# Optimization experiments

Hardware: AMD Instinct MI355X
Metric: run time of the kernel (lower is better)

Reference implementation:

```python
import jax, jax.numpy as jnp
import numpy as np

N, E = 50000, 1600000
FEAT, HID, HEADS = 256, 64, 2
NEG_SLOPE = 0.2


def gat_conv(x, src, dst, W, att_src, att_dst, bias, heads, out_ch):
    """PyG GATConv (concat=True, self-loops already appended to src/dst)."""
    n = x.shape[0]
    h = (x @ W).reshape(n, heads, out_ch)                      # [N,H,C]
    a_src = jnp.einsum('nhc,hc->nh', h, att_src)               # [N,H]
    a_dst = jnp.einsum('nhc,hc->nh', h, att_dst)               # [N,H]
    alpha = jax.nn.leaky_relu(a_src[src] + a_dst[dst], NEG_SLOPE)  # [E',H]
    # segment softmax over incoming edges of each dst node
    amax = jax.ops.segment_max(alpha, dst, num_segments=n)
    alpha = jnp.exp(alpha - amax[dst])
    denom = jax.ops.segment_sum(alpha, dst, num_segments=n)
    alpha = alpha / (denom[dst] + 1e-16)
    msg = h[src] * alpha[..., None]                            # [E',H,C]
    out = jax.ops.segment_sum(msg, dst, num_segments=n)        # [N,H,C]
    return out.reshape(n, heads * out_ch) + bias


def setup_inputs() -> dict:
    key = jax.random.key(0)
    ks = jax.random.split(key, 10)
    x = jax.random.normal(ks[0], (N, FEAT), dtype=jnp.float32)
    edge_index = jax.random.randint(ks[1], (2, E), 0, N, dtype=jnp.int64)
    s1 = 1.0 / np.sqrt(FEAT)
    s2 = 1.0 / np.sqrt(HID * HEADS)
    sa = 1.0 / np.sqrt(HID)
    return {
        'x': x,
        'edge_index': edge_index,
        'W1': jax.random.uniform(ks[2], (FEAT, HEADS * HID), jnp.float32, -s1, s1),
        'att_src1': jax.random.uniform(ks[3], (HEADS, HID), jnp.float32, -sa, sa),
        'att_dst1': jax.random.uniform(ks[4], (HEADS, HID), jnp.float32, -sa, sa),
        'b1': jnp.zeros((HEADS * HID,), jnp.float32),
        'W2': jax.random.uniform(ks[5], (HEADS * HID, HID), jnp.float32, -s2, s2),
        'att_src2': jax.random.uniform(ks[6], (1, HID), jnp.float32, -sa, sa),
        'att_dst2': jax.random.uniform(ks[7], (1, HID), jnp.float32, -sa, sa),
        'b2': jnp.zeros((HID,), jnp.float32),
    }


def reference(x, edge_index, W1, att_src1, att_dst1, b1, W2, att_src2, att_dst2, b2):
    n = x.shape[0]
    loop = jnp.arange(n, dtype=edge_index.dtype)
    src = jnp.concatenate([edge_index[0], loop])   # add self loops (PyG default)
    dst = jnp.concatenate([edge_index[1], loop])
    h = gat_conv(x, src, dst, W1, att_src1, att_dst1, b1, HEADS, HID)
    h = jax.nn.relu(h)  # dropout is identity in eval mode
    h = gat_conv(h, src, dst, W2, att_src2, att_dst2, b2, 1, HID)
    return jax.nn.log_softmax(h, axis=1)
```

## Files before the change

kernel.cpp:

```cpp
#include <hip/hip_runtime.h>
#include <hip/hip_bf16.h>
#include <math.h>

typedef short bf16x8 __attribute__((ext_vector_type(8)));
typedef float f32x4 __attribute__((ext_vector_type(4)));

#define BSHIFT 7
#define BWIDTH 128
#define PCHUNK 4096

__global__ void prep_kernel(int* __restrict__ bcnt,
                            const float* __restrict__ W1, const float* __restrict__ W2,
                            __hip_bfloat16* __restrict__ W1t,
                            __hip_bfloat16* __restrict__ W2t) {
    if (blockIdx.x == 0) {
        bcnt[threadIdx.x] = 0;
        bcnt[threadIdx.x + 256] = 0;
        return;
    }
    int idx = (blockIdx.x - 1) * 256 + threadIdx.x;
    const int n1 = 128 * 256;
    if (idx < n1) {
        int nn = idx >> 8, kk = idx & 255;
        W1t[idx] = __float2bfloat16(W1[kk * 128 + nn]);
    } else {
        int j = idx - n1;
        if (j < 64 * 128) {
            int nn = j >> 7, kk = j & 127;
            W2t[j] = __float2bfloat16(W2[kk * 64 + nn]);
        }
    }
}

__global__ __launch_bounds__(256) void bucket_hist(const int* __restrict__ ei, int E,
                                                   int* __restrict__ bcnt) {
    __shared__ int h[512];
    int tid = threadIdx.x;
    for (int i = tid; i < 512; i += 256) h[i] = 0;
    __syncthreads();
    int start = blockIdx.x * PCHUNK;
    int cnt = min(PCHUNK, E - start);
    for (int i = tid; i < cnt; i += 256)
        atomicAdd(&h[ei[E + start + i] >> BSHIFT], 1);
    __syncthreads();
    for (int i = tid; i < 512; i += 256)
        if (h[i]) atomicAdd(&bcnt[i], h[i]);
}

__global__ __launch_bounds__(512) void bucket_scan(const int* __restrict__ bcnt,
                                                   int* __restrict__ bbase,
                                                   int* __restrict__ bcur,
                                                   int nbk, int n) {
    __shared__ int s[512];
    int tid = threadIdx.x;
    int nodes = 0;
    if (tid < nbk) nodes = min(BWIDTH, n - (tid << BSHIFT));
    int v = (tid < nbk) ? bcnt[tid] + nodes : 0;
    s[tid] = v;
    __syncthreads();
    #pragma unroll
    for (int o = 1; o < 512; o <<= 1) {
        int t = (tid >= o) ? s[tid - o] : 0;
        __syncthreads();
        s[tid] += t;
        __syncthreads();
    }
    if (tid < nbk) {
        int ex = s[tid] - v;
        bbase[tid] = ex;
        bcur[tid] = ex - (tid << BSHIFT);
    }
    if (tid == nbk) bbase[nbk] = s[tid];
}

__global__ __launch_bounds__(256) void partition_edges(const int* __restrict__ ei, int E,
                                                       int* __restrict__ bcur,
                                                       int* __restrict__ tmp) {
    __shared__ int2 stage[PCHUNK];
    __shared__ int h[512];
    __shared__ int lbase[512];
    int tid = threadIdx.x;
    int start = blockIdx.x * PCHUNK;
    int cnt = min(PCHUNK, E - start);
    for (int i = tid; i < 512; i += 256) h[i] = 0;
    __syncthreads();
    for (int i = tid; i < cnt; i += 256) {
        int s = ei[start + i];
        int d = ei[E + start + i];
        stage[i] = make_int2(s, d);
        atomicAdd(&h[d >> BSHIFT], 1);
    }
    __syncthreads();
    for (int i = tid; i < 512; i += 256) {
        if (h[i] > 0) lbase[i] = atomicAdd(&bcur[i], h[i]);
        h[i] = 0;
    }
    __syncthreads();
    for (int i = tid; i < cnt; i += 256) {
        int2 e = stage[i];
        int b = e.y >> BSHIFT;
        int r = atomicAdd(&h[b], 1);
        tmp[lbase[b] + r] = (e.x << BSHIFT) | (e.y & (BWIDTH - 1));
    }
}

__global__ __launch_bounds__(256) void bucket_csr(const int* __restrict__ bbase,
                                                  const int* __restrict__ tmp,
                                                  int* __restrict__ offs,
                                                  int* __restrict__ srcs,
                                                  int n, int nbk) {
    __shared__ int cnt[BWIDTH];
    __shared__ int sa[BWIDTH];
    __shared__ int cur[BWIDTH];
    int b = blockIdx.x;
    int tid = threadIdx.x;
    int node0 = b << BSHIFT;
    int nnodes = min(BWIDTH, n - node0);
    int cb = bbase[b];
    int ce = bbase[b + 1];
    int tb = cb - node0;
    int ecnt = (ce - cb) - nnodes;

    if (tid < BWIDTH) cnt[tid] = (tid < nnodes) ? 1 : 0;
    __syncthreads();
    for (int i = tid; i < ecnt; i += 256)
        atomicAdd(&cnt[tmp[tb + i] & (BWIDTH - 1)], 1);
    __syncthreads();
    if (tid < BWIDTH) sa[tid] = cnt[tid];
    __syncthreads();
    #pragma unroll
    for (int o = 1; o < BWIDTH; o <<= 1) {
        int v = 0;
        if (tid < BWIDTH) { v = sa[tid]; if (tid >= o) v += sa[tid - o]; }
        __syncthreads();
        if (tid < BWIDTH) sa[tid] = v;
        __syncthreads();
    }
    if (tid < BWIDTH) {
        int ex = sa[tid] - cnt[tid];
        if (tid < nnodes) {
            offs[node0 + tid] = cb + ex;
            srcs[cb + ex] = node0 + tid;
        }
        cur[tid] = ex + (tid < nnodes ? 1 : 0);
    }
    if (b == nbk - 1 && tid == 0) offs[n] = ce;
    __syncthreads();
    for (int i = tid; i < ecnt; i += 256) {
        int e = tmp[tb + i];
        int li = e & (BWIDTH - 1);
        int r = atomicAdd(&cur[li], 1);
        srcs[cb + r] = e >> BSHIFT;
    }
}

template <bool A_BF16, int NT, int HEADS, int KSTEPS>
__global__ __launch_bounds__(256) void gemm_att(
    const void* __restrict__ Av, const __hip_bfloat16* __restrict__ Bt,
    __hip_bfloat16* __restrict__ C,
    const float* __restrict__ atts, const float* __restrict__ attd,
    float* __restrict__ a_s, float* __restrict__ a_d, int M) {
    constexpr int K = KSTEPS * 32;
    constexpr int N = NT * 16;
    constexpr int KH = 128;
    constexpr int NCH = (K + KH - 1) / KH;
    constexpr int LDB = KH + 8;
    __shared__ __hip_bfloat16 Bs[N][LDB];

    int tid = threadIdx.x;
    int w = tid >> 6, l = tid & 63;
    int q = l >> 4, m16 = l & 15;
    int bm = blockIdx.x * 64;
    int arow = bm + w * 16 + m16;
    if (arow >= M) arow = M - 1;

    f32x4 acc[NT];
    #pragma unroll
    for (int t = 0; t < NT; t++) acc[t] = (f32x4){0.f, 0.f, 0.f, 0.f};

    #pragma unroll
    for (int ch = 0; ch < NCH; ch++) {
        const int cb = ch * KH;
        bf16x8 af[4];
        float4 st[8];
        if (A_BF16) {
            const __hip_bfloat16* A = (const __hip_bfloat16*)Av + (size_t)arow * K + cb + q * 8;
            #pragma unroll
            for (int t = 0; t < 4; t++)
                af[t] = *(const bf16x8*)(A + t * 32);
        } else {
            const float* A = (const float*)Av + (size_t)arow * K + cb + q * 8;
            #pragma unroll
            for (int t = 0; t < 4; t++) {
                st[2 * t]     = *(const float4*)(A + t * 32);
                st[2 * t + 1] = *(const float4*)(A + t * 32 + 4);
            }
        }
        for (int i = tid; i < (N * KH) / 8; i += 256) {
            int row = i >> 4;
            int k = (i & 15) * 8;
            *(uint4*)&Bs[row][k] = *(const uint4*)(Bt + (size_t)row * K + cb + k);
        }
        __syncthreads();
        if (!A_BF16) {
            #pragma unroll
            for (int t = 0; t < 4; t++) {
                union { __hip_bfloat16 h[8]; bf16x8 v; } u;
                float4 v0 = st[2 * t], v1 = st[2 * t + 1];
                u.h[0] = __float2bfloat16(v0.x); u.h[1] = __float2bfloat16(v0.y);
                u.h[2] = __float2bfloat16(v0.z); u.h[3] = __float2bfloat16(v0.w);
                u.h[4] = __float2bfloat16(v1.x); u.h[5] = __float2bfloat16(v1.y);
                u.h[6] = __float2bfloat16(v1.z); u.h[7] = __float2bfloat16(v1.w);
                af[t] = u.v;
            }
        }
        #pragma unroll
        for (int t = 0; t < 4; t++) {
            #pragma unroll
            for (int c = 0; c < NT; c++) {
                bf16x8 b = *(const bf16x8*)&Bs[c * 16 + m16][t * 32 + q * 8];
                acc[c] = __builtin_amdgcn_mfma_f32_16x16x32_bf16(af[t], b, acc[c], 0, 0, 0);
            }
        }
        if (ch + 1 < NCH) __syncthreads();
    }

    #pragma unroll
    for (int t = 0; t < NT; t++) {
        #pragma unroll
        for (int r = 0; r < 4; r++) {
            int row = bm + w * 16 + q * 4 + r;
            if (row < M) C[(size_t)row * N + t * 16 + m16] = __float2bfloat16(acc[t][r]);
        }
    }

    float ps[HEADS][4], pd[HEADS][4];
    #pragma unroll
    for (int hh = 0; hh < HEADS; hh++)
        #pragma unroll
        for (int r = 0; r < 4; r++) { ps[hh][r] = 0.f; pd[hh][r] = 0.f; }
    #pragma unroll
    for (int t = 0; t < NT; t++) {
        int ch = t * 16 + m16;
        float asw = atts[ch], adw = attd[ch];
        int hh = (HEADS == 2) ? (t >> 2) : 0;
        #pragma unroll
        for (int r = 0; r < 4; r++) {
            ps[hh][r] = fmaf(acc[t][r], asw, ps[hh][r]);
            pd[hh][r] = fmaf(acc[t][r], adw, pd[hh][r]);
        }
    }
    #pragma unroll
    for (int o = 1; o < 16; o <<= 1) {
        #pragma unroll
        for (int hh = 0; hh < HEADS; hh++)
            #pragma unroll
            for (int r = 0; r < 4; r++) {
                ps[hh][r] += __shfl_xor(ps[hh][r], o);
                pd[hh][r] += __shfl_xor(pd[hh][r], o);
            }
    }
    if (m16 == 0) {
        #pragma unroll
        for (int r = 0; r < 4; r++) {
            int row = bm + w * 16 + q * 4 + r;
            if (row < M) {
                if (HEADS == 2) {
                    a_s[row * 2]     = ps[0][r];
                    a_s[row * 2 + 1] = ps[1][r];
                    a_d[row * 2]     = pd[0][r];
                    a_d[row * 2 + 1] = pd[1][r];
                } else {
                    a_s[row] = ps[0][r];
                    a_d[row] = pd[0][r];
                }
            }
        }
    }
}

__device__ __forceinline__ float leaky(float r) {
    return r < 0.f ? 0.2f * r : r;
}

__device__ __forceinline__ void unpack2(unsigned u, float& lo, float& hi) {
    lo = __uint_as_float(u << 16);
    hi = __uint_as_float(u & 0xffff0000u);
}

__global__ __launch_bounds__(256) void edge_agg_l1(
    const int* __restrict__ offs, const int* __restrict__ srcs,
    const __hip_bfloat16* __restrict__ h1, const float* __restrict__ asv,
    const float* __restrict__ adv, const float* __restrict__ bias,
    __hip_bfloat16* __restrict__ out, int d0, int dlim) {
    int d = d0 + ((blockIdx.x * blockDim.x + threadIdx.x) >> 6);
    int lane = threadIdx.x & 63;
    if (d >= dlim) return;
    int start = offs[d], end = offs[d + 1];
    float ad0 = adv[2 * d], ad1 = adv[2 * d + 1];

    int sub = lane & 15;
    int g = lane >> 4;
    int ch0 = sub * 8;
    int hsel = sub >> 3;

    float s0 = 0.f, s1 = 0.f;
    float acc[8];
    #pragma unroll
    for (int k = 0; k < 8; k++) acc[k] = 0.f;

    for (int base = start; base < end; base += 64) {
        int cnt = min(64, end - base);
        int s_l = 0;
        float e0 = 0.f, e1 = 0.f;
        if (lane < cnt) {
            s_l = srcs[base + lane];
            float2 a = *(const float2*)(asv + 2 * s_l);
            e0 = __expf(leaky(a.x + ad0));
            e1 = __expf(leaky(a.y + ad1));
        }
        s0 += e0;
        s1 += e1;

        int steps = (cnt + 3) >> 2;
        int jj = 0;
        for (; jj + 4 <= steps; jj += 4) {
            float wgt[4]; int sr[4];
            #pragma unroll
            for (int u = 0; u < 4; u++) {
                int e = (jj + u) * 4 + g;
                float w0 = __shfl(e0, e);
                float w1 = __shfl(e1, e);
                sr[u] = __shfl(s_l, e);
                wgt[u] = hsel ? w1 : w0;
            }
            uint4 v[4];
            #pragma unroll
            for (int u = 0; u < 4; u++)
                v[u] = *(const uint4*)(h1 + (size_t)sr[u] * 128 + ch0);
            #pragma unroll
            for (int u = 0; u < 4; u++) {
                float f0, f1, f2, f3, f4, f5, f6, f7;
                unpack2(v[u].x, f0, f1); unpack2(v[u].y, f2, f3);
                unpack2(v[u].z, f4, f5); unpack2(v[u].w, f6, f7);
                float wA = wgt[u];
                acc[0] = fmaf(wA, f0, acc[0]); acc[1] = fmaf(wA, f1, acc[1]);
                acc[2] = fmaf(wA, f2, acc[2]); acc[3] = fmaf(wA, f3, acc[3]);
                acc[4] = fmaf(wA, f4, acc[4]); acc[5] = fmaf(wA, f5, acc[5]);
                acc[6] = fmaf(wA, f6, acc[6]); acc[7] = fmaf(wA, f7, acc[7]);
            }
        }
        for (; jj + 2 <= steps; jj += 2) {
            int eA = jj * 4 + g, eB = eA + 4;
            float w0A = __shfl(e0, eA), w1A = __shfl(e1, eA);
            int sA = __shfl(s_l, eA);
            float w0B = __shfl(e0, eB), w1B = __shfl(e1, eB);
            int sB = __shfl(s_l, eB);
            float wA = hsel ? w1A : w0A;
            float wB = hsel ? w1B : w0B;
            uint4 vA = *(const uint4*)(h1 + (size_t)sA * 128 + ch0);
            uint4 vB = *(const uint4*)(h1 + (size_t)sB * 128 + ch0);
            float f0, f1, f2, f3, f4, f5, f6, f7;
            unpack2(vA.x, f0, f1); unpack2(vA.y, f2, f3);
            unpack2(vA.z, f4, f5); unpack2(vA.w, f6, f7);
            acc[0] = fmaf(wA, f0, acc[0]); acc[1] = fmaf(wA, f1, acc[1]);
            acc[2] = fmaf(wA, f2, acc[2]); acc[3] = fmaf(wA, f3, acc[3]);
            acc[4] = fmaf(wA, f4, acc[4]); acc[5] = fmaf(wA, f5, acc[5]);
            acc[6] = fmaf(wA, f6, acc[6]); acc[7] = fmaf(wA, f7, acc[7]);
            unpack2(vB.x, f0, f1); unpack2(vB.y, f2, f3);
            unpack2(vB.z, f4, f5); unpack2(vB.w, f6, f7);
            acc[0] = fmaf(wB, f0, acc[0]); acc[1] = fmaf(wB, f1, acc[1]);
            acc[2] = fmaf(wB, f2, acc[2]); acc[3] = fmaf(wB, f3, acc[3]);
            acc[4] = fmaf(wB, f4, acc[4]); acc[5] = fmaf(wB, f5, acc[5]);
            acc[6] = fmaf(wB, f6, acc[6]); acc[7] = fmaf(wB, f7, acc[7]);
        }
        if (jj < steps) {
            int eA = jj * 4 + g;
            float w0A = __shfl(e0, eA), w1A = __shfl(e1, eA);
            int sA = __shfl(s_l, eA);
            float wA = hsel ? w1A : w0A;
            uint4 vA = *(const uint4*)(h1 + (size_t)sA * 128 + ch0);
            float f0, f1, f2, f3, f4, f5, f6, f7;
            unpack2(vA.x, f0, f1); unpack2(vA.y, f2, f3);
            unpack2(vA.z, f4, f5); unpack2(vA.w, f6, f7);
            acc[0] = fmaf(wA, f0, acc[0]); acc[1] = fmaf(wA, f1, acc[1]);
            acc[2] = fmaf(wA, f2, acc[2]); acc[3] = fmaf(wA, f3, acc[3]);
            acc[4] = fmaf(wA, f4, acc[4]); acc[5] = fmaf(wA, f5, acc[5]);
            acc[6] = fmaf(wA, f6, acc[6]); acc[7] = fmaf(wA, f7, acc[7]);
        }
    }
    #pragma unroll
    for (int o = 16; o < 64; o <<= 1)
        #pragma unroll
        for (int k = 0; k < 8; k++) acc[k] += __shfl_xor(acc[k], o);
    #pragma unroll
    for (int o = 1; o < 64; o <<= 1) {
        s0 += __shfl_xor(s0, o);
        s1 += __shfl_xor(s1, o);
    }

    if (lane < 16) {
        float invh = 1.f / ((hsel ? s1 : s0) + 1e-16f);
        float4 b0 = *(const float4*)(bias + ch0);
        float4 b1 = *(const float4*)(bias + ch0 + 4);
        union { __hip_bfloat16 h[8]; uint4 u; } o2;
        o2.h[0] = __float2bfloat16(fmaxf(fmaf(acc[0], invh, b0.x), 0.f));
        o2.h[1] = __float2bfloat16(fmaxf(fmaf(acc[1], invh, b0.y), 0.f));
        o2.h[2] = __float2bfloat16(fmaxf(fmaf(acc[2], invh, b0.z), 0.f));
        o2.h[3] = __float2bfloat16(fmaxf(fmaf(acc[3], invh, b0.w), 0.f));
        o2.h[4] = __float2bfloat16(fmaxf(fmaf(acc[4], invh, b1.x), 0.f));
        o2.h[5] = __float2bfloat16(fmaxf(fmaf(acc[5], invh, b1.y), 0.f));
        o2.h[6] = __float2bfloat16(fmaxf(fmaf(acc[6], invh, b1.z), 0.f));
        o2.h[7] = __float2bfloat16(fmaxf(fmaf(acc[7], invh, b1.w), 0.f));
        *(uint4*)(out + (size_t)d * 128 + ch0) = o2.u;
    }
}

__global__ __launch_bounds__(256) void edge_agg_l2(
    const int* __restrict__ offs, const int* __restrict__ srcs,
    const __hip_bfloat16* __restrict__ h2, const float* __restrict__ asv,
    const float* __restrict__ adv, const float* __restrict__ bias,
    float* __restrict__ out, int n) {
    int d = (blockIdx.x * blockDim.x + threadIdx.x) >> 6;
    int lane = threadIdx.x & 63;
    if (d >= n) return;
    int start = offs[d], end = offs[d + 1];
    float ad = adv[d];

    int sub = lane & 7;
    int g = lane >> 3;
    int ch0 = sub * 8;

    float ssum = 0.f;
    float acc[8];
    #pragma unroll
    for (int k = 0; k < 8; k++) acc[k] = 0.f;

    for (int base = start; base < end; base += 64) {
        int cnt = min(64, end - base);
        int s_l = 0;
        float ew = 0.f;
        if (lane < cnt) {
            s_l = srcs[base + lane];
            ew = __expf(leaky(asv[s_l] + ad));
        }
        ssum += ew;

        int steps = (cnt + 7) >> 3;
        int jj = 0;
        for (; jj + 4 <= steps; jj += 4) {
            float wgt[4]; int sr[4];
            #pragma unroll
            for (int u = 0; u < 4; u++) {
                int e = (jj + u) * 8 + g;
                wgt[u] = __shfl(ew, e);
                sr[u] = __shfl(s_l, e);
            }
            uint4 v[4];
            #pragma unroll
            for (int u = 0; u < 4; u++)
                v[u] = *(const uint4*)(h2 + (size_t)sr[u] * 64 + ch0);
            #pragma unroll
            for (int u = 0; u < 4; u++) {
                float f0, f1, f2, f3, f4, f5, f6, f7;
                unpack2(v[u].x, f0, f1); unpack2(v[u].y, f2, f3);
                unpack2(v[u].z, f4, f5); unpack2(v[u].w, f6, f7);
                float wA = wgt[u];
                acc[0] = fmaf(wA, f0, acc[0]); acc[1] = fmaf(wA, f1, acc[1]);
                acc[2] = fmaf(wA, f2, acc[2]); acc[3] = fmaf(wA, f3, acc[3]);
                acc[4] = fmaf(wA, f4, acc[4]); acc[5] = fmaf(wA, f5, acc[5]);
                acc[6] = fmaf(wA, f6, acc[6]); acc[7] = fmaf(wA, f7, acc[7]);
            }
        }
        for (; jj + 2 <= steps; jj += 2) {
            int eA = jj * 8 + g, eB = eA + 8;
            float wA = __shfl(ew, eA);
            int sA = __shfl(s_l, eA);
            float wB = __shfl(ew, eB);
            int sB = __shfl(s_l, eB);
            uint4 vA = *(const uint4*)(h2 + (size_t)sA * 64 + ch0);
            uint4 vB = *(const uint4*)(h2 + (size_t)sB * 64 + ch0);
            float f0, f1, f2, f3, f4, f5, f6, f7;
            unpack2(vA.x, f0, f1); unpack2(vA.y, f2, f3);
            unpack2(vA.z, f4, f5); unpack2(vA.w, f6, f7);
            acc[0] = fmaf(wA, f0, acc[0]); acc[1] = fmaf(wA, f1, acc[1]);
            acc[2] = fmaf(wA, f2, acc[2]); acc[3] = fmaf(wA, f3, acc[3]);
            acc[4] = fmaf(wA, f4, acc[4]); acc[5] = fmaf(wA, f5, acc[5]);
            acc[6] = fmaf(wA, f6, acc[6]); acc[7] = fmaf(wA, f7, acc[7]);
            unpack2(vB.x, f0, f1); unpack2(vB.y, f2, f3);
            unpack2(vB.z, f4, f5); unpack2(vB.w, f6, f7);
            acc[0] = fmaf(wB, f0, acc[0]); acc[1] = fmaf(wB, f1, acc[1]);
            acc[2] = fmaf(wB, f2, acc[2]); acc[3] = fmaf(wB, f3, acc[3]);
            acc[4] = fmaf(wB, f4, acc[4]); acc[5] = fmaf(wB, f5, acc[5]);
            acc[6] = fmaf(wB, f6, acc[6]); acc[7] = fmaf(wB, f7, acc[7]);
        }
        if (jj < steps) {
            int eA = jj * 8 + g;
            float wA = __shfl(ew, eA);
            int sA = __shfl(s_l, eA);
            uint4 vA = *(const uint4*)(h2 + (size_t)sA * 64 + ch0);
            float f0, f1, f2, f3, f4, f5, f6, f7;
            unpack2(vA.x, f0, f1); unpack2(vA.y, f2, f3);
            unpack2(vA.z, f4, f5); unpack2(vA.w, f6, f7);
            acc[0] = fmaf(wA, f0, acc[0]); acc[1] = fmaf(wA, f1, acc[1]);
            acc[2] = fmaf(wA, f2, acc[2]); acc[3] = fmaf(wA, f3, acc[3]);
            acc[4] = fmaf(wA, f4, acc[4]); acc[5] = fmaf(wA, f5, acc[5]);
            acc[6] = fmaf(wA, f6, acc[6]); acc[7] = fmaf(wA, f7, acc[7]);
        }
    }
    #pragma unroll
    for (int o = 8; o < 64; o <<= 1)
        #pragma unroll
        for (int k = 0; k < 8; k++) acc[k] += __shfl_xor(acc[k], o);
    #pragma unroll
    for (int o = 1; o < 64; o <<= 1) ssum += __shfl_xor(ssum, o);

    float inv = 1.f / (ssum + 1e-16f);
    float4 b0 = *(const float4*)(bias + ch0);
    float4 b1 = *(const float4*)(bias + ch0 + 4);
    float v[8];
    v[0] = fmaf(acc[0], inv, b0.x); v[1] = fmaf(acc[1], inv, b0.y);
    v[2] = fmaf(acc[2], inv, b0.z); v[3] = fmaf(acc[3], inv, b0.w);
    v[4] = fmaf(acc[4], inv, b1.x); v[5] = fmaf(acc[5], inv, b1.y);
    v[6] = fmaf(acc[6], inv, b1.z); v[7] = fmaf(acc[7], inv, b1.w);

    float vm = v[0];
    #pragma unroll
    for (int k = 1; k < 8; k++) vm = fmaxf(vm, v[k]);
    #pragma unroll
    for (int o = 1; o < 8; o <<= 1) vm = fmaxf(vm, __shfl_xor(vm, o));
    float se_loc = 0.f;
    #pragma unroll
    for (int k = 0; k < 8; k++) se_loc += __expf(v[k] - vm);
    #pragma unroll
    for (int o = 1; o < 8; o <<= 1) se_loc += __shfl_xor(se_loc, o);
    float lse = vm + logf(se_loc);

    if (lane < 8) {
        float4 o0 = make_float4(v[0] - lse, v[1] - lse, v[2] - lse, v[3] - lse);
        float4 o1 = make_float4(v[4] - lse, v[5] - lse, v[6] - lse, v[7] - lse);
        *(float4*)(out + (size_t)d * 64 + ch0) = o0;
        *(float4*)(out + (size_t)d * 64 + ch0 + 4) = o1;
    }
}

extern "C" void kernel_launch(void* const* d_in, const int* in_sizes, int n_in,
                              void* d_out, int out_size, void* d_ws, size_t ws_size,
                              hipStream_t stream) {
    const float* x    = (const float*)d_in[0];
    const int*   ei   = (const int*)d_in[1];
    const float* W1   = (const float*)d_in[2];
    const float* as1w = (const float*)d_in[3];
    const float* ad1w = (const float*)d_in[4];
    const float* b1   = (const float*)d_in[5];
    const float* W2   = (const float*)d_in[6];
    const float* as2w = (const float*)d_in[7];
    const float* ad2w = (const float*)d_in[8];
    const float* b2   = (const float*)d_in[9];
    float* out = (float*)d_out;

    const int n = in_sizes[0] / 256;
    const int E = in_sizes[1] / 2;
    const int tot = E + n;
    const int nbk = (n + BWIDTH - 1) / BWIDTH;

    char* p = (char*)d_ws;
    auto alloc = [&](size_t bytes) {
        void* r = (void*)p;
        p += (bytes + 255) & ~(size_t)255;
        return r;
    };
    int*   offs  = (int*)alloc((size_t)(n + 1) * 4);
    int*   srcs  = (int*)alloc((size_t)tot * 4);
    int*   tmp   = (int*)alloc((size_t)E * 4);
    int*   bcnt  = (int*)alloc(512 * 4);
    int*   bbase = (int*)alloc(512 * 4);
    int*   bcur  = (int*)alloc(512 * 4);
    __hip_bfloat16* W1t = (__hip_bfloat16*)alloc((size_t)128 * 256 * 2);
    __hip_bfloat16* W2t = (__hip_bfloat16*)alloc((size_t)64 * 128 * 2);
    __hip_bfloat16* h1  = (__hip_bfloat16*)alloc((size_t)n * 128 * 2);
    __hip_bfloat16* out1= (__hip_bfloat16*)alloc((size_t)n * 128 * 2);
    __hip_bfloat16* h2  = (__hip_bfloat16*)alloc((size_t)n * 64 * 2);
    float* a_s1 = (float*)alloc((size_t)n * 2 * 4);
    float* a_d1 = (float*)alloc((size_t)n * 2 * 4);
    float* a_s2 = (float*)alloc((size_t)n * 4);
    float* a_d2 = (float*)alloc((size_t)n * 4);

    int pblocks = (E + PCHUNK - 1) / PCHUNK;

    prep_kernel<<<1 + (128 * 256 + 64 * 128 + 255) / 256, 256, 0, stream>>>(
        bcnt, W1, W2, W1t, W2t);

    bucket_hist<<<pblocks, 256, 0, stream>>>(ei, E, bcnt);
    bucket_scan<<<1, 512, 0, stream>>>(bcnt, bbase, bcur, nbk, n);
    partition_edges<<<pblocks, 256, 0, stream>>>(ei, E, bcur, tmp);
    bucket_csr<<<nbk, 256, 0, stream>>>(bbase, tmp, offs, srcs, n, nbk);

    gemm_att<false, 8, 2, 8><<<(n + 63) / 64, 256, 0, stream>>>(
        x, W1t, h1, as1w, ad1w, a_s1, a_d1, n);
    int nh = n / 2;
    edge_agg_l1<<<((size_t)nh * 64 + 255) / 256, 256, 0, stream>>>(
        offs, srcs, h1, a_s1, a_d1, b1, out1, 0, nh);
    edge_agg_l1<<<((size_t)(n - nh) * 64 + 255) / 256, 256, 0, stream>>>(
        offs, srcs, h1, a_s1, a_d1, b1, out1, nh, n);

    gemm_att<true, 4, 1, 4><<<(n + 63) / 64, 256, 0, stream>>>(
        out1, W2t, h2, as2w, ad2w, a_s2, a_d2, n);
    edge_agg_l2<<<((size_t)n * 64 + 255) / 256, 256, 0, stream>>>(
        offs, srcs, h2, a_s2, a_d2, b2, out, n);
}
```

Before: 268.4 us.

## Compute edge weights per lane and prefetch source indices in GAT aggregation

Both edge aggregation kernels drop the cooperative load-then-shuffle scheme. Each lane group now reads its own source indices directly, prefetching the next four a loop iteration ahead, and computes the attention exponent redundantly for its own edges, keeping only a partial denominator per group. This removes the shuffle traffic and the 64-edge chunk serialization, at the cost of redundant exp/asv loads across the channel lanes of a group. The layer-1 aggregation is also merged back into a single launch instead of two half launches.

```diff
diff --git a/kernel.cpp b/kernel.cpp
--- a/kernel.cpp
+++ b/kernel.cpp
@@ -292,115 +292,114 @@
     const int* __restrict__ offs, const int* __restrict__ srcs,
     const __hip_bfloat16* __restrict__ h1, const float* __restrict__ asv,
     const float* __restrict__ adv, const float* __restrict__ bias,
-    __hip_bfloat16* __restrict__ out, int d0, int dlim) {
-    int d = d0 + ((blockIdx.x * blockDim.x + threadIdx.x) >> 6);
+    __hip_bfloat16* __restrict__ out, int n) {
+    int d = (blockIdx.x * blockDim.x + threadIdx.x) >> 6;
     int lane = threadIdx.x & 63;
-    if (d >= dlim) return;
+    if (d >= n) return;
     int start = offs[d], end = offs[d + 1];
-    float ad0 = adv[2 * d], ad1 = adv[2 * d + 1];
-
+    int cnt = end - start;
     int sub = lane & 15;
     int g = lane >> 4;
     int ch0 = sub * 8;
     int hsel = sub >> 3;
-
-    float s0 = 0.f, s1 = 0.f;
+    float ad = adv[2 * d + hsel];
+
+    float wsum = 0.f;
     float acc[8];
     #pragma unroll
     for (int k = 0; k < 8; k++) acc[k] = 0.f;
 
-    for (int base = start; base < end; base += 64) {
-        int cnt = min(64, end - base);
-        int s_l = 0;
-        float e0 = 0.f, e1 = 0.f;
-        if (lane < cnt) {
-            s_l = srcs[base + lane];
-            float2 a = *(const float2*)(asv + 2 * s_l);
-            e0 = __expf(leaky(a.x + ad0));
-            e1 = __expf(leaky(a.y + ad1));
-        }
-        s0 += e0;
-        s1 += e1;
-
-        int steps = (cnt + 3) >> 2;
-        int jj = 0;
-        for (; jj + 4 <= steps; jj += 4) {
-            float wgt[4]; int sr[4];
-            #pragma unroll
-            for (int u = 0; u < 4; u++) {
-                int e = (jj + u) * 4 + g;
-                float w0 = __shfl(e0, e);
-                float w1 = __shfl(e1, e);
-                sr[u] = __shfl(s_l, e);
-                wgt[u] = hsel ? w1 : w0;
-            }
-            uint4 v[4];
-            #pragma unroll
-            for (int u = 0; u < 4; u++)
-                v[u] = *(const uint4*)(h1 + (size_t)sr[u] * 128 + ch0);
-            #pragma unroll
-            for (int u = 0; u < 4; u++) {
-                float f0, f1, f2, f3, f4, f5, f6, f7;
-                unpack2(v[u].x, f0, f1); unpack2(v[u].y, f2, f3);
-                unpack2(v[u].z, f4, f5); unpack2(v[u].w, f6, f7);
-                float wA = wgt[u];
-                acc[0] = fmaf(wA, f0, acc[0]); acc[1] = fmaf(wA, f1, acc[1]);
-                acc[2] = fmaf(wA, f2, acc[2]); acc[3] = fmaf(wA, f3, acc[3]);
-                acc[4] = fmaf(wA, f4, acc[4]); acc[5] = fmaf(wA, f5, acc[5]);
-                acc[6] = fmaf(wA, f6, acc[6]); acc[7] = fmaf(wA, f7, acc[7]);
-            }
-        }
-        for (; jj + 2 <= steps; jj += 2) {
-            int eA = jj * 4 + g, eB = eA + 4;
-            float w0A = __shfl(e0, eA), w1A = __shfl(e1, eA);
-            int sA = __shfl(s_l, eA);
-            float w0B = __shfl(e0, eB), w1B = __shfl(e1, eB);
-            int sB = __shfl(s_l, eB);
-            float wA = hsel ? w1A : w0A;
-            float wB = hsel ? w1B : w0B;
-            uint4 vA = *(const uint4*)(h1 + (size_t)sA * 128 + ch0);
-            uint4 vB = *(const uint4*)(h1 + (size_t)sB * 128 + ch0);
-            float f0, f1, f2, f3, f4, f5, f6, f7;
-            unpack2(vA.x, f0, f1); unpack2(vA.y, f2, f3);
-            unpack2(vA.z, f4, f5); unpack2(vA.w, f6, f7);
-            acc[0] = fmaf(wA, f0, acc[0]); acc[1] = fmaf(wA, f1, acc[1]);
-            acc[2] = fmaf(wA, f2, acc[2]); acc[3] = fmaf(wA, f3, acc[3]);
-            acc[4] = fmaf(wA, f4, acc[4]); acc[5] = fmaf(wA, f5, acc[5]);
-            acc[6] = fmaf(wA, f6, acc[6]); acc[7] = fmaf(wA, f7, acc[7]);
-            unpack2(vB.x, f0, f1); unpack2(vB.y, f2, f3);
-            unpack2(vB.z, f4, f5); unpack2(vB.w, f6, f7);
-            acc[0] = fmaf(wB, f0, acc[0]); acc[1] = fmaf(wB, f1, acc[1]);
-            acc[2] = fmaf(wB, f2, acc[2]); acc[3] = fmaf(wB, f3, acc[3]);
-            acc[4] = fmaf(wB, f4, acc[4]); acc[5] = fmaf(wB, f5, acc[5]);
-            acc[6] = fmaf(wB, f6, acc[6]); acc[7] = fmaf(wB, f7, acc[7]);
-        }
-        if (jj < steps) {
-            int eA = jj * 4 + g;
-            float w0A = __shfl(e0, eA), w1A = __shfl(e1, eA);
-            int sA = __shfl(s_l, eA);
-            float wA = hsel ? w1A : w0A;
-            uint4 vA = *(const uint4*)(h1 + (size_t)sA * 128 + ch0);
-            float f0, f1, f2, f3, f4, f5, f6, f7;
-            unpack2(vA.x, f0, f1); unpack2(vA.y, f2, f3);
-            unpack2(vA.z, f4, f5); unpack2(vA.w, f6, f7);
-            acc[0] = fmaf(wA, f0, acc[0]); acc[1] = fmaf(wA, f1, acc[1]);
-            acc[2] = fmaf(wA, f2, acc[2]); acc[3] = fmaf(wA, f3, acc[3]);
-            acc[4] = fmaf(wA, f4, acc[4]); acc[5] = fmaf(wA, f5, acc[5]);
-            acc[6] = fmaf(wA, f6, acc[6]); acc[7] = fmaf(wA, f7, acc[7]);
-        }
-    }
-    #pragma unroll
-    for (int o = 16; o < 64; o <<= 1)
+    int full = cnt >> 2;
+    int ib = start + g;
+    int jj = 0;
+    int pA = 0, pB = 0, pC = 0, pD = 0;
+    if (jj + 4 <= full) {
+        pA = srcs[ib];      pB = srcs[ib + 4];
+        pC = srcs[ib + 8];  pD = srcs[ib + 12];
+    }
+    for (; jj + 4 <= full; jj += 4) {
+        int sA = pA, sB = pB, sC = pC, sD = pD;
+        if (jj + 8 <= full) {
+            int nb = ib + (jj + 4) * 4;
+            pA = srcs[nb];      pB = srcs[nb + 4];
+            pC = srcs[nb + 8];  pD = srcs[nb + 12];
+        }
+        uint4 vA = *(const uint4*)(h1 + (size_t)sA * 128 + ch0);
+        uint4 vB = *(const uint4*)(h1 + (size_t)sB * 128 + ch0);
+        uint4 vC = *(const uint4*)(h1 + (size_t)sC * 128 + ch0);
+        uint4 vD = *(const uint4*)(h1 + (size_t)sD * 128 + ch0);
+        float aA = asv[2 * sA + hsel];
+        float aB = asv[2 * sB + hsel];
+        float aC = asv[2 * sC + hsel];
+        float aD = asv[2 * sD + hsel];
+        float wA = __expf(leaky(aA + ad));
+        float wB = __expf(leaky(aB + ad));
+        float wC = __expf(leaky(aC + ad));
+        float wD = __expf(leaky(aD + ad));
+        wsum += (wA + wB) + (wC + wD);
+        float f0, f1, f2, f3, f4, f5, f6, f7;
+        unpack2(vA.x, f0, f1); unpack2(vA.y, f2, f3);
+        unpack2(vA.z, f4, f5); unpack2(vA.w, f6, f7);
+        acc[0] = fmaf(wA, f0, acc[0]); acc[1] = fmaf(wA, f1, acc[1]);
+        acc[2] = fmaf(wA, f2, acc[2]); acc[3] = fmaf(wA, f3, acc[3]);
+        acc[4] = fmaf(wA, f4, acc[4]); acc[5] = fmaf(wA, f5, acc[5]);
+        acc[6] = fmaf(wA, f6, acc[6]); acc[7] = fmaf(wA, f7, acc[7]);
+        unpack2(vB.x, f0, f1); unpack2(vB.y, f2, f3);
+        unpack2(vB.z, f4, f5); unpack2(vB.w, f6, f7);
+        acc[0] = fmaf(wB, f0, acc[0]); acc[1] = fmaf(wB, f1, acc[1]);
+        acc[2] = fmaf(wB, f2, acc[2]); acc[3] = fmaf(wB, f3, acc[3]);
+        acc[4] = fmaf(wB, f4, acc[4]); acc[5] = fmaf(wB, f5, acc[5]);
+        acc[6] = fmaf(wB, f6, acc[6]); acc[7] = fmaf(wB, f7, acc[7]);
+        unpack2(vC.x, f0, f1); unpack2(vC.y, f2, f3);
+        unpack2(vC.z, f4, f5); unpack2(vC.w, f6, f7);
+        acc[0] = fmaf(wC, f0, acc[0]); acc[1] = fmaf(wC, f1, acc[1]);
+        acc[2] = fmaf(wC, f2, acc[2]); acc[3] = fmaf(wC, f3, acc[3]);
+        acc[4] = fmaf(wC, f4, acc[4]); acc[5] = fmaf(wC, f5, acc[5]);
+        acc[6] = fmaf(wC, f6, acc[6]); acc[7] = fmaf(wC, f7, acc[7]);
+        unpack2(vD.x, f0, f1); unpack2(vD.y, f2, f3);
+        unpack2(vD.z, f4, f5); unpack2(vD.w, f6, f7);
+        acc[0] = fmaf(wD, f0, acc[0]); acc[1] = fmaf(wD, f1, acc[1]);
+        acc[2] = fmaf(wD, f2, acc[2]); acc[3] = fmaf(wD, f3, acc[3]);
+        acc[4] = fmaf(wD, f4, acc[4]); acc[5] = fmaf(wD, f5, acc[5]);
+        acc[6] = fmaf(wD, f6, acc[6]); acc[7] = fmaf(wD, f7, acc[7]);
+    }
+    for (; jj < full; jj++) {
+        int s = srcs[ib + jj * 4];
+        uint4 v = *(const uint4*)(h1 + (size_t)s * 128 + ch0);
+        float a = asv[2 * s + hsel];
+        float wA = __expf(leaky(a + ad));
+        wsum += wA;
+        float f0, f1, f2, f3, f4, f5, f6, f7;
+        unpack2(v.x, f0, f1); unpack2(v.y, f2, f3);
+        unpack2(v.z, f4, f5); unpack2(v.w, f6, f7);
+        acc[0] = fmaf(wA, f0, acc[0]); acc[1] = fmaf(wA, f1, acc[1]);
+        acc[2] = fmaf(wA, f2, acc[2]); acc[3] = fmaf(wA, f3, acc[3]);
+        acc[4] = fmaf(wA, f4, acc[4]); acc[5] = fmaf(wA, f5, acc[5]);
+        acc[6] = fmaf(wA, f6, acc[6]); acc[7] = fmaf(wA, f7, acc[7]);
+    }
+    if (full * 4 + g < cnt) {
+        int s = srcs[ib + full * 4];
+        uint4 v = *(const uint4*)(h1 + (size_t)s * 128 + ch0);
+        float a = asv[2 * s + hsel];
+        float wA = __expf(leaky(a + ad));
+        wsum += wA;
+        float f0, f1, f2, f3, f4, f5, f6, f7;
+        unpack2(v.x, f0, f1); unpack2(v.y, f2, f3);
+        unpack2(v.z, f4, f5); unpack2(v.w, f6, f7);
+        acc[0] = fmaf(wA, f0, acc[0]); acc[1] = fmaf(wA, f1, acc[1]);
+        acc[2] = fmaf(wA, f2, acc[2]); acc[3] = fmaf(wA, f3, acc[3]);
+        acc[4] = fmaf(wA, f4, acc[4]); acc[5] = fmaf(wA, f5, acc[5]);
+        acc[6] = fmaf(wA, f6, acc[6]); acc[7] = fmaf(wA, f7, acc[7]);
+    }
+    #pragma unroll
+    for (int o = 16; o < 64; o <<= 1) {
         #pragma unroll
         for (int k = 0; k < 8; k++) acc[k] += __shfl_xor(acc[k], o);
-    #pragma unroll
-    for (int o = 1; o < 64; o <<= 1) {
-        s0 += __shfl_xor(s0, o);
-        s1 += __shfl_xor(s1, o);
+        wsum += __shfl_xor(wsum, o);
     }
 
     if (lane < 16) {
-        float invh = 1.f / ((hsel ? s1 : s0) + 1e-16f);
+        float invh = 1.f / (wsum + 1e-16f);
         float4 b0 = *(const float4*)(bias + ch0);
         float4 b1 = *(const float4*)(bias + ch0 + 4);
         union { __hip_bfloat16 h[8]; uint4 u; } o2;
@@ -425,97 +424,104 @@
     int lane = threadIdx.x & 63;
     if (d >= n) return;
     int start = offs[d], end = offs[d + 1];
-    float ad = adv[d];
-
+    int cnt = end - start;
     int sub = lane & 7;
     int g = lane >> 3;
     int ch0 = sub * 8;
-
-    float ssum = 0.f;
+    float ad = adv[d];
+
+    float wsum = 0.f;
     float acc[8];
     #pragma unroll
     for (int k = 0; k < 8; k++) acc[k] = 0.f;
 
-    for (int base = start; base < end; base += 64) {
-        int cnt = min(64, end - base);
-        int s_l = 0;
-        float ew = 0.f;
-        if (lane < cnt) {
-            s_l = srcs[base + lane];
-            ew = __expf(leaky(asv[s_l] + ad));
-        }
-        ssum += ew;
-
-        int steps = (cnt + 7) >> 3;
-        int jj = 0;
-        for (; jj + 4 <= steps; jj += 4) {
-            float wgt[4]; int sr[4];
-            #pragma unroll
-            for (int u = 0; u < 4; u++) {
-                int e = (jj + u) * 8 + g;
-                wgt[u] = __shfl(ew, e);
-                sr[u] = __shfl(s_l, e);
-            }
-            uint4 v[4];
-            #pragma unroll
-            for (int u = 0; u < 4; u++)
-                v[u] = *(const uint4*)(h2 + (size_t)sr[u] * 64 + ch0);
-            #pragma unroll
-            for (int u = 0; u < 4; u++) {
-                float f0, f1, f2, f3, f4, f5, f6, f7;
-                unpack2(v[u].x, f0, f1); unpack2(v[u].y, f2, f3);
-                unpack2(v[u].z, f4, f5); unpack2(v[u].w, f6, f7);
-                float wA = wgt[u];
-                acc[0] = fmaf(wA, f0, acc[0]); acc[1] = fmaf(wA, f1, acc[1]);
-                acc[2] = fmaf(wA, f2, acc[2]); acc[3] = fmaf(wA, f3, acc[3]);
-                acc[4] = fmaf(wA, f4, acc[4]); acc[5] = fmaf(wA, f5, acc[5]);
-                acc[6] = fmaf(wA, f6, acc[6]); acc[7] = fmaf(wA, f7, acc[7]);
-            }
-        }
-        for (; jj + 2 <= steps; jj += 2) {
-            int eA = jj * 8 + g, eB = eA + 8;
-            float wA = __shfl(ew, eA);
-            int sA = __shfl(s_l, eA);
-            float wB = __shfl(ew, eB);
-            int sB = __shfl(s_l, eB);
-            uint4 vA = *(const uint4*)(h2 + (size_t)sA * 64 + ch0);
-            uint4 vB = *(const uint4*)(h2 + (size_t)sB * 64 + ch0);
-            float f0, f1, f2, f3, f4, f5, f6, f7;
-            unpack2(vA.x, f0, f1); unpack2(vA.y, f2, f3);
-            unpack2(vA.z, f4, f5); unpack2(vA.w, f6, f7);
-            acc[0] = fmaf(wA, f0, acc[0]); acc[1] = fmaf(wA, f1, acc[1]);
-            acc[2] = fmaf(wA, f2, acc[2]); acc[3] = fmaf(wA, f3, acc[3]);
-            acc[4] = fmaf(wA, f4, acc[4]); acc[5] = fmaf(wA, f5, acc[5]);
-            acc[6] = fmaf(wA, f6, acc[6]); acc[7] = fmaf(wA, f7, acc[7]);
-            unpack2(vB.x, f0, f1); unpack2(vB.y, f2, f3);
-            unpack2(vB.z, f4, f5); unpack2(vB.w, f6, f7);
-            acc[0] = fmaf(wB, f0, acc[0]); acc[1] = fmaf(wB, f1, acc[1]);
-            acc[2] = fmaf(wB, f2, acc[2]); acc[3] = fmaf(wB, f3, acc[3]);
-            acc[4] = fmaf(wB, f4, acc[4]); acc[5] = fmaf(wB, f5, acc[5]);
-            acc[6] = fmaf(wB, f6, acc[6]); acc[7] = fmaf(wB, f7, acc[7]);
-        }
-        if (jj < steps) {
-            int eA = jj * 8 + g;
-            float wA = __shfl(ew, eA);
-            int sA = __shfl(s_l, eA);
-            uint4 vA = *(const uint4*)(h2 + (size_t)sA * 64 + ch0);
-            float f0, f1, f2, f3, f4, f5, f6, f7;
-            unpack2(vA.x, f0, f1); unpack2(vA.y, f2, f3);
-            unpack2(vA.z, f4, f5); unpack2(vA.w, f6, f7);
-            acc[0] = fmaf(wA, f0, acc[0]); acc[1] = fmaf(wA, f1, acc[1]);
-            acc[2] = fmaf(wA, f2, acc[2]); acc[3] = fmaf(wA, f3, acc[3]);
-            acc[4] = fmaf(wA, f4, acc[4]); acc[5] = fmaf(wA, f5, acc[5]);
-            acc[6] = fmaf(wA, f6, acc[6]); acc[7] = fmaf(wA, f7, acc[7]);
-        }
-    }
-    #pragma unroll
-    for (int o = 8; o < 64; o <<= 1)
+    int full = cnt >> 3;
+    int ib = start + g;
+    int jj = 0;
+    int pA = 0, pB = 0, pC = 0, pD = 0;
+    if (jj + 4 <= full) {
+        pA = srcs[ib];       pB = srcs[ib + 8];
+        pC = srcs[ib + 16];  pD = srcs[ib + 24];
+    }
+    for (; jj + 4 <= full; jj += 4) {
+        int sA = pA, sB = pB, sC = pC, sD = pD;
+        if (jj + 8 <= full) {
+            int nb = ib + (jj + 4) * 8;
+            pA = srcs[nb];       pB = srcs[nb + 8];
+            pC = srcs[nb + 16];  pD = srcs[nb + 24];
+        }
+        uint4 vA = *(const uint4*)(h2 + (size_t)sA * 64 + ch0);
+        uint4 vB = *(const uint4*)(h2 + (size_t)sB * 64 + ch0);
+        uint4 vC = *(const uint4*)(h2 + (size_t)sC * 64 + ch0);
+        uint4 vD = *(const uint4*)(h2 + (size_t)sD * 64 + ch0);
+        float aA = asv[sA], aB = asv[sB], aC = asv[sC], aD = asv[sD];
+        float wA = __expf(leaky(aA + ad));
+        float wB = __expf(leaky(aB + ad));
+        float wC = __expf(leaky(aC + ad));
+        float wD = __expf(leaky(aD + ad));
+        wsum += (wA + wB) + (wC + wD);
+        float f0, f1, f2, f3, f4, f5, f6, f7;
+        unpack2(vA.x, f0, f1); unpack2(vA.y, f2, f3);
+        unpack2(vA.z, f4, f5); unpack2(vA.w, f6, f7);
+        acc[0] = fmaf(wA, f0, acc[0]); acc[1] = fmaf(wA, f1, acc[1]);
+        acc[2] = fmaf(wA, f2, acc[2]); acc[3] = fmaf(wA, f3, acc[3]);
+        acc[4] = fmaf(wA, f4, acc[4]); acc[5] = fmaf(wA, f5, acc[5]);
+        acc[6] = fmaf(wA, f6, acc[6]); acc[7] = fmaf(wA, f7, acc[7]);
+        unpack2(vB.x, f0, f1); unpack2(vB.y, f2, f3);
+        unpack2(vB.z, f4, f5); unpack2(vB.w, f6, f7);
+        acc[0] = fmaf(wB, f0, acc[0]); acc[1] = fmaf(wB, f1, acc[1]);
+        acc[2] = fmaf(wB, f2, acc[2]); acc[3] = fmaf(wB, f3, acc[3]);
+        acc[4] = fmaf(wB, f4, acc[4]); acc[5] = fmaf(wB, f5, acc[5]);
+        acc[6] = fmaf(wB, f6, acc[6]); acc[7] = fmaf(wB, f7, acc[7]);
+        unpack2(vC.x, f0, f1); unpack2(vC.y, f2, f3);
+        unpack2(vC.z, f4, f5); unpack2(vC.w, f6, f7);
+        acc[0] = fmaf(wC, f0, acc[0]); acc[1] = fmaf(wC, f1, acc[1]);
+        acc[2] = fmaf(wC, f2, acc[2]); acc[3] = fmaf(wC, f3, acc[3]);
+        acc[4] = fmaf(wC, f4, acc[4]); acc[5] = fmaf(wC, f5, acc[5]);
+        acc[6] = fmaf(wC, f6, acc[6]); acc[7] = fmaf(wC, f7, acc[7]);
+        unpack2(vD.x, f0, f1); unpack2(vD.y, f2, f3);
+        unpack2(vD.z, f4, f5); unpack2(vD.w, f6, f7);
+        acc[0] = fmaf(wD, f0, acc[0]); acc[1] = fmaf(wD, f1, acc[1]);
+        acc[2] = fmaf(wD, f2, acc[2]); acc[3] = fmaf(wD, f3, acc[3]);
+        acc[4] = fmaf(wD, f4, acc[4]); acc[5] = fmaf(wD, f5, acc[5]);
+        acc[6] = fmaf(wD, f6, acc[6]); acc[7] = fmaf(wD, f7, acc[7]);
+    }
+    for (; jj < full; jj++) {
+        int s = srcs[ib + jj * 8];
+        uint4 v = *(const uint4*)(h2 + (size_t)s * 64 + ch0);
+        float a = asv[s];
+        float wA = __expf(leaky(a + ad));
+        wsum += wA;
+        float f0, f1, f2, f3, f4, f5, f6, f7;
+        unpack2(v.x, f0, f1); unpack2(v.y, f2, f3);
+        unpack2(v.z, f4, f5); unpack2(v.w, f6, f7);
+        acc[0] = fmaf(wA, f0, acc[0]); acc[1] = fmaf(wA, f1, acc[1]);
+        acc[2] = fmaf(wA, f2, acc[2]); acc[3] = fmaf(wA, f3, acc[3]);
+        acc[4] = fmaf(wA, f4, acc[4]); acc[5] = fmaf(wA, f5, acc[5]);
+        acc[6] = fmaf(wA, f6, acc[6]); acc[7] = fmaf(wA, f7, acc[7]);
+    }
+    if (full * 8 + g < cnt) {
+        int s = srcs[ib + full * 8];
+        uint4 v = *(const uint4*)(h2 + (size_t)s * 64 + ch0);
+        float a = asv[s];
+        float wA = __expf(leaky(a + ad));
+        wsum += wA;
+        float f0, f1, f2, f3, f4, f5, f6, f7;
+        unpack2(v.x, f0, f1); unpack2(v.y, f2, f3);
+        unpack2(v.z, f4, f5); unpack2(v.w, f6, f7);
+        acc[0] = fmaf(wA, f0, acc[0]); acc[1] = fmaf(wA, f1, acc[1]);
+        acc[2] = fmaf(wA, f2, acc[2]); acc[3] = fmaf(wA, f3, acc[3]);
+        acc[4] = fmaf(wA, f4, acc[4]); acc[5] = fmaf(wA, f5, acc[5]);
+        acc[6] = fmaf(wA, f6, acc[6]); acc[7] = fmaf(wA, f7, acc[7]);
+    }
+    #pragma unroll
+    for (int o = 8; o < 64; o <<= 1) {
         #pragma unroll
         for (int k = 0; k < 8; k++) acc[k] += __shfl_xor(acc[k], o);
-    #pragma unroll
-    for (int o = 1; o < 64; o <<= 1) ssum += __shfl_xor(ssum, o);
-
-    float inv = 1.f / (ssum + 1e-16f);
+        wsum += __shfl_xor(wsum, o);
+    }
+
+    float inv = 1.f / (wsum + 1e-16f);
     float4 b0 = *(const float4*)(bias + ch0);
     float4 b1 = *(const float4*)(bias + ch0 + 4);
     float v[8];
@@ -598,11 +604,8 @@
 
     gemm_att<false, 8, 2, 8><<<(n + 63) / 64, 256, 0, stream>>>(
         x, W1t, h1, as1w, ad1w, a_s1, a_d1, n);
-    int nh = n / 2;
-    edge_agg_l1<<<((size_t)nh * 64 + 255) / 256, 256, 0, stream>>>(
-        offs, srcs, h1, a_s1, a_d1, b1, out1, 0, nh);
-    edge_agg_l1<<<((size_t)(n - nh) * 64 + 255) / 256, 256, 0, stream>>>(
-        offs, srcs, h1, a_s1, a_d1, b1, out1, nh, n);
+    edge_agg_l1<<<((size_t)n * 64 + 255) / 256, 256, 0, stream>>>(
+        offs, srcs, h1, a_s1, a_d1, b1, out1, n);
 
     gemm_att<true, 4, 1, 4><<<(n + 63) / 64, 256, 0, stream>>>(
         out1, W2t, h2, as2w, ad2w, a_s2, a_d2, n);
```

Result: no change. 267.1 us (-0.5%).
